# Kernel optimization log

Measured on AMD Instinct MI355X. Metric: run time of the kernel, lower is better.

## Reference

```python
import jax, jax.numpy as jnp
import numpy as np

B, T, S, H, E = 4, 2048, 2048, 16, 64  # batch, q_len, kv_len, heads, head_dim


def setup_inputs() -> dict:
    key = jax.random.key(0)
    kq, kk, kv, kl, kw = jax.random.split(key, 5)
    query = jax.random.normal(kq, (B, T, H * E), dtype=jnp.float32)
    key_t = jax.random.normal(kk, (B, S, H * E), dtype=jnp.float32)
    value = jax.random.normal(kv, (B, S, H * E), dtype=jnp.float32)
    # valid lengths in [S//2, S] so every row has at least one attendable key
    lengths = jax.random.randint(kl, (B,), S // 2, S + 1)
    key_padding_mask = jnp.arange(S)[None, :] < lengths[:, None]  # (B, S) bool, True = keep
    W_out = jax.random.normal(kw, (H * E, E), dtype=jnp.float32) * 0.02
    b_out = jnp.zeros((E,), dtype=jnp.float32)
    return {"query": query, "key": key_t, "value": value,
            "key_padding_mask": key_padding_mask, "W_out": W_out, "b_out": b_out}


def reference(query, key, value, key_padding_mask, W_out, b_out):
    # (B, N, H*E) -> (B, H, N, E)
    q = query.reshape(B, T, H, E).transpose(0, 2, 1, 3)
    k = key.reshape(B, S, H, E).transpose(0, 2, 1, 3)
    v = value.reshape(B, S, H, E).transpose(0, 2, 1, 3)
    softmax_temp = 1.0 / np.sqrt(E).astype(np.float32)
    scores = jnp.einsum('bhte,bhse->bhts', q * softmax_temp, k)  # (B,H,T,S)
    neg_inf = jnp.finfo(scores.dtype).min
    scores = jnp.where(key_padding_mask[:, None, None, :], scores, neg_inf)
    attn = jax.nn.softmax(scores, axis=-1)  # dropout p=0 -> identity
    out = jnp.einsum('bhts,bhsd->bthd', attn, v)  # (B,T,H,E)
    out = out.reshape(B * T, H * E)
    return out @ W_out + b_out  # (B*T, E)
```

## Files before the change

### kernel.cpp

```cpp
#include <hip/hip_runtime.h>
#include <hip/hip_bf16.h>

#define Bq 4
#define Tq 2048
#define Sq 2048
#define Hq 16
#define Eq 64
#define HEq 1024

typedef __attribute__((ext_vector_type(8))) _Float16 half8;
typedef __attribute__((ext_vector_type(16))) float f32x16;

#define AS1 __attribute__((address_space(1)))
#define AS3 __attribute__((address_space(3)))

__device__ __forceinline__ void gl_lds16(const void* g, void* l) {
  __builtin_amdgcn_global_load_lds((const AS1 unsigned*)g, (AS3 unsigned*)l, 16, 0, 0);
}
#define VMCNT(n) asm volatile("s_waitcnt vmcnt(" #n ")" ::: "memory")
#define LGKM0 asm volatile("s_waitcnt lgkmcnt(0)" ::: "memory")

#if __has_builtin(__builtin_amdgcn_exp2f)
#define EXP2F(x) __builtin_amdgcn_exp2f(x)
#else
#define EXP2F(x) exp2f(x)
#endif

__device__ __forceinline__ unsigned pk16(float a, float b) {
  return __builtin_bit_cast(unsigned, __builtin_amdgcn_cvt_pkrtz(a, b));
}

__global__ __launch_bounds__(256) void prep_kernel(
    const float* __restrict__ K, const float* __restrict__ V,
    const float* __restrict__ W, const void* __restrict__ mask,
    char* __restrict__ KP, char* __restrict__ VP,
    _Float16* __restrict__ WT, int* __restrict__ lens) {
  __shared__ _Float16 tile[64][72];
  const int bid = blockIdx.x;
  const int tid = threadIdx.x;

  if (bid < 4096) {
    const int isV = bid >= 2048;
    const int b2 = bid & 2047;
    const int t = b2 & 31, h = (b2 >> 5) & 15, b = b2 >> 9;
    const int s0 = t * 64;
    const int s_in = tid >> 2, e0 = (tid & 3) * 16;
    const float* X = isV ? V : K;
    const float* src = X + ((size_t)(b * Sq + s0 + s_in) * HEq + h * Eq + e0);
#pragma unroll
    for (int i = 0; i < 4; ++i) {
      const float4 f = *(const float4*)(src + i * 4);
      tile[s_in][e0 + i * 4 + 0] = (_Float16)f.x;
      tile[s_in][e0 + i * 4 + 1] = (_Float16)f.y;
      tile[s_in][e0 + i * 4 + 2] = (_Float16)f.z;
      tile[s_in][e0 + i * 4 + 3] = (_Float16)f.w;
    }
    __syncthreads();
    half8 u0, u1;
    if (!isV) {
      const int gi = tid >> 5, sl = (tid & 31) * 2;
#pragma unroll
      for (int j = 0; j < 8; ++j) {
        u0[j] = tile[sl][gi * 8 + j];
        u1[j] = tile[sl + 1][gi * 8 + j];
      }
      char* dst = KP + ((size_t)b2 * 8192) + tid * 32;
      *(half8*)dst = u0;
      *(half8*)(dst + 16) = u1;
    } else {
      const int sgi = tid >> 5, e = (tid & 31) * 2;
#pragma unroll
      for (int j = 0; j < 8; ++j) {
        u0[j] = tile[sgi * 8 + j][e];
        u1[j] = tile[sgi * 8 + j][e + 1];
      }
      char* dst = VP + ((size_t)b2 * 8192) + tid * 32;
      *(half8*)dst = u0;
      *(half8*)(dst + 16) = u1;
    }
  } else if (bid < 4352) {
    const int id = (bid - 4096) * 256 + tid;
    const int n = id >> 10, k = id & 1023;
    WT[id] = (_Float16)W[k * Eq + n];
  } else if (tid < 64) {
    const int b = bid - 4352;
    const int lane = tid;
    const unsigned w0 = *(const unsigned*)mask;
    int cnt = 0;
    if (w0 == 1u) {
      const int* m = (const int*)mask + b * Sq;
      for (int s = lane; s < Sq; s += 64) cnt += (m[s] != 0);
    } else if (w0 == 0x3F800000u) {
      const float* m = (const float*)mask + b * Sq;
      for (int s = lane; s < Sq; s += 64) cnt += (m[s] != 0.f);
    } else {
      const unsigned char* m = (const unsigned char*)mask + b * Sq;
      for (int s = lane; s < Sq; s += 64) cnt += (m[s] != 0);
    }
    for (int o = 32; o; o >>= 1) cnt += __shfl_down(cnt, o);
    if (lane == 0) lens[b] = cnt;
  }
}

__global__ __launch_bounds__(512, 4) void flash_kernel(
    const float* __restrict__ Q, const char* __restrict__ KP,
    const char* __restrict__ VP, const int* __restrict__ lens,
    _Float16* __restrict__ attnO) {
  __shared__ __align__(16) _Float16 KV[2][2][4096];

  const int bid = blockIdx.x;
  const int qt = bid >> 6;
  const int h = (bid >> 2) & 15;
  const int b = ((bid & 3) + (bid >> 8)) & 3;
  const int tid = threadIdx.x;
  const int w = tid >> 6, lane = tid & 63;
  const int qq = lane & 31, hi = lane >> 5;
  const int len = lens[b];
  const int q0 = qt * 256 + w * 32;

  const float qscale = 0.125f * 1.44269504088896340736f;
  half8 qf[4];
  {
    const float* qrow = Q + ((size_t)(b * Tq + q0 + qq) * HEq + h * Eq);
#pragma unroll
    for (int kw = 0; kw < 4; ++kw) {
      const float4 f0 = *(const float4*)(qrow + kw * 16 + hi * 8);
      const float4 f1 = *(const float4*)(qrow + kw * 16 + hi * 8 + 4);
      half8 qv;
      qv[0] = (_Float16)(f0.x * qscale);
      qv[1] = (_Float16)(f0.y * qscale);
      qv[2] = (_Float16)(f0.z * qscale);
      qv[3] = (_Float16)(f0.w * qscale);
      qv[4] = (_Float16)(f1.x * qscale);
      qv[5] = (_Float16)(f1.y * qscale);
      qv[6] = (_Float16)(f1.z * qscale);
      qv[7] = (_Float16)(f1.w * qscale);
      qf[kw] = qv;
    }
  }

  f32x16 Oa[2];
#pragma unroll
  for (int i = 0; i < 2; ++i)
#pragma unroll
    for (int r = 0; r < 16; ++r) Oa[i][r] = 0.f;
  float ls0 = 0.f, ls1 = 0.f;

  const char* kpb = KP + (size_t)(b * Hq + h) * 32 * 8192;
  const char* vpb = VP + (size_t)(b * Hq + h) * 32 * 8192;
  const int so = w * 1024 + lane * 16;

  const int ntiles = (len + 63) >> 6;

  gl_lds16(kpb + so, (char*)&KV[0][0][0] + so);
  gl_lds16(vpb + so, (char*)&KV[0][1][0] + so);

  int p = 0;
  for (int t = 0; t < ntiles; ++t) {
    if (t + 1 < ntiles) {
      const size_t tb = (size_t)(t + 1) * 8192;
      gl_lds16(kpb + tb + so, (char*)&KV[p ^ 1][0][0] + so);
      gl_lds16(vpb + tb + so, (char*)&KV[p ^ 1][1][0] + so);
      VMCNT(2);
    } else {
      VMCNT(0);
    }
    __builtin_amdgcn_s_barrier();
    __builtin_amdgcn_sched_barrier(0);

    __builtin_amdgcn_s_setprio(1);
    f32x16 sc[2];
#pragma unroll
    for (int sm = 0; sm < 2; ++sm) {
      f32x16 acc;
#pragma unroll
      for (int r = 0; r < 16; ++r) acc[r] = 0.f;
#pragma unroll
      for (int kw = 0; kw < 4; ++kw) {
        const half8 kf = *(const half8*)((const char*)&KV[p][0][0] +
                                         (kw * 2 + hi) * 1024 + (sm * 32 + qq) * 16);
        acc = __builtin_amdgcn_mfma_f32_32x32x16_f16(kf, qf[kw], acc, 0, 0, 0);
      }
      sc[sm] = acc;
    }
    __builtin_amdgcn_s_setprio(0);

    const int svalid = len - (t << 6);
    if (svalid < 64) {
#pragma unroll
      for (int r = 0; r < 16; ++r) {
        const int sl = (r & 3) + 8 * (r >> 2) + 4 * hi;
        if (sl >= svalid) sc[0][r] = -60000.f;
        if (32 + sl >= svalid) sc[1][r] = -60000.f;
      }
    }

    unsigned pku[2][4][2];
#pragma unroll
    for (int sm = 0; sm < 2; ++sm)
#pragma unroll
      for (int rb = 0; rb < 4; ++rb)
#pragma unroll
        for (int pp = 0; pp < 2; ++pp) {
          const float a0 = EXP2F(sc[sm][rb * 4 + pp * 2]);
          const float a1 = EXP2F(sc[sm][rb * 4 + pp * 2 + 1]);
          ls0 += a0;
          ls1 += a1;
          pku[sm][rb][pp] = pk16(a0, a1);
        }

#pragma unroll
    for (int kw = 0; kw < 4; ++kw) {
      const int sm = kw >> 1;
      const int rbe = (kw & 1) * 2, rbo = rbe + 1;
      union { unsigned u[4]; half8 h; } pu;
#pragma unroll
      for (int pp = 0; pp < 2; ++pp) {
        const unsigned ev = pku[sm][rbe][pp];
        const unsigned od = pku[sm][rbo][pp];
        const unsigned sendv = hi ? ev : od;
        const unsigned recvv = __shfl_xor(sendv, 32);
        pu.u[pp] = hi ? recvv : ev;
        pu.u[2 + pp] = hi ? od : recvv;
      }
      const half8 pf = pu.h;
      __builtin_amdgcn_s_setprio(1);
#pragma unroll
      for (int eh = 0; eh < 2; ++eh) {
        const half8 vf = *(const half8*)((const char*)&KV[p][1][0] +
                                         (kw * 2 + hi) * 1024 + (eh * 32 + qq) * 16);
        Oa[eh] = __builtin_amdgcn_mfma_f32_32x32x16_f16(vf, pf, Oa[eh], 0, 0, 0);
      }
      __builtin_amdgcn_s_setprio(0);
    }

    __builtin_amdgcn_s_barrier();
    __builtin_amdgcn_sched_barrier(0);
    p ^= 1;
  }

  float ls = ls0 + ls1;
  ls += __shfl_xor(ls, 32);
  const float inv = 1.f / ls;
  char* const scratch = (char*)&KV[0][0][0] + w * 4096;
#pragma unroll
  for (int eh = 0; eh < 2; ++eh)
#pragma unroll
    for (int rb = 0; rb < 4; ++rb)
#pragma unroll
      for (int pp = 0; pp < 2; ++pp) {
        const int e0 = eh * 32 + rb * 8 + hi * 4 + pp * 2;
        const unsigned uo = pk16(Oa[eh][rb * 4 + pp * 2] * inv,
                                 Oa[eh][rb * 4 + pp * 2 + 1] * inv);
        *(unsigned*)(scratch + qq * 128 + ((e0 * 2) ^ ((qq & 7) << 4))) = uo;
      }
  LGKM0;
  __builtin_amdgcn_sched_barrier(0);
#pragma unroll
  for (int i = 0; i < 4; ++i) {
    const int qr = i * 8 + (lane >> 3), ch = lane & 7;
    const half8 ov = *(const half8*)(scratch + qr * 128 + ((ch * 16) ^ ((qr & 7) << 4)));
    *(half8*)(attnO + (size_t)(b * Tq + q0 + qr) * HEq + h * Eq + ch * 8) = ov;
  }
}

typedef __attribute__((ext_vector_type(4))) float floatx4;
__global__ __launch_bounds__(256) void proj_kernel(
    const _Float16* __restrict__ A, const _Float16* __restrict__ WT,
    const float* __restrict__ bias, float* __restrict__ out) {
  const int tid = threadIdx.x;
  const int w = tid >> 6, lane = tid & 63;
  const int g = lane >> 4, c = lane & 15;
  const int r0 = blockIdx.x * 64 + w * 16;
  floatx4 acc[4];
#pragma unroll
  for (int i = 0; i < 4; ++i) acc[i] = (floatx4){0.f, 0.f, 0.f, 0.f};
  const _Float16* arow = A + (size_t)(r0 + c) * HEq;
  for (int kc = 0; kc < 32; ++kc) {
    const half8 af = *(const half8*)(arow + kc * 32 + g * 8);
#pragma unroll
    for (int nt = 0; nt < 4; ++nt) {
      const half8 bf =
          *(const half8*)(WT + (size_t)(nt * 16 + c) * HEq + kc * 32 + g * 8);
      acc[nt] = __builtin_amdgcn_mfma_f32_16x16x32_f16(af, bf, acc[nt], 0, 0, 0);
    }
  }
#pragma unroll
  for (int r = 0; r < 4; ++r) {
    const int row = r0 + g * 4 + r;
#pragma unroll
    for (int nt = 0; nt < 4; ++nt) {
      const int col = nt * 16 + c;
      out[(size_t)row * Eq + col] = acc[nt][r] + bias[col];
    }
  }
}

extern "C" void kernel_launch(void* const* d_in, const int* in_sizes, int n_in,
                              void* d_out, int out_size, void* d_ws, size_t ws_size,
                              hipStream_t stream) {
  const float* q = (const float*)d_in[0];
  const float* k = (const float*)d_in[1];
  const float* v = (const float*)d_in[2];
  const void* mask = d_in[3];
  const float* W = (const float*)d_in[4];
  const float* bias = (const float*)d_in[5];
  float* out = (float*)d_out;

  char* ws = (char*)d_ws;
  int* lens = (int*)ws;
  _Float16* WT = (_Float16*)(ws + 256);
  _Float16* attn = (_Float16*)(ws + (256 + 131072));
  char* KP = ws + (256 + 131072 + (1 << 24));
  char* VP = ws + (256 + 131072 + (1 << 24) + (1 << 24));

  prep_kernel<<<4356, 256, 0, stream>>>(k, v, W, mask, KP, VP, WT, lens);
  flash_kernel<<<512, 512, 0, stream>>>(q, KP, VP, lens, attn);
  proj_kernel<<<(Bq * Tq) / 64, 256, 0, stream>>>(attn, WT, bias, out);
}
```

Measured before the change: 108.4 us.

## Process two KV tiles per barrier and compute softmax row sums via MFMA

The KV loop now stages two 64-key tiles per buffer half, so each barrier pair covers two tiles and loads run further ahead. That doubles LDS use to 64KB per block, which may limit occupancy. The per-lane scalar accumulation of exp values plus the cross-lane shuffle for the row sum is replaced by an extra MFMA against a ones vector, which yields the row sums in an accumulator. This removes VALU adds but adds one MFMA per k-step, and the sum is now taken over fp16-rounded probabilities.

Result: slower. 113.4 us (+4.6%).

```diff
diff --git a/kernel.cpp b/kernel.cpp
--- a/kernel.cpp
+++ b/kernel.cpp
@@ -106,7 +106,7 @@
     const float* __restrict__ Q, const char* __restrict__ KP,
     const char* __restrict__ VP, const int* __restrict__ lens,
     _Float16* __restrict__ attnO) {
-  __shared__ __align__(16) _Float16 KV[2][2][4096];
+  __shared__ __align__(16) _Float16 KV[2][2][2][4096];
 
   const int bid = blockIdx.x;
   const int qt = bid >> 6;
@@ -139,35 +139,25 @@
     }
   }
 
-  f32x16 Oa[2];
+  half8 ones;
+#pragma unroll
+  for (int j = 0; j < 8; ++j) ones[j] = (_Float16)1.0f;
+
+  f32x16 Oa[2], La;
 #pragma unroll
   for (int i = 0; i < 2; ++i)
 #pragma unroll
     for (int r = 0; r < 16; ++r) Oa[i][r] = 0.f;
-  float ls0 = 0.f, ls1 = 0.f;
+#pragma unroll
+  for (int r = 0; r < 16; ++r) La[r] = 0.f;
 
   const char* kpb = KP + (size_t)(b * Hq + h) * 32 * 8192;
   const char* vpb = VP + (size_t)(b * Hq + h) * 32 * 8192;
   const int so = w * 1024 + lane * 16;
 
-  const int ntiles = (len + 63) >> 6;
-
-  gl_lds16(kpb + so, (char*)&KV[0][0][0] + so);
-  gl_lds16(vpb + so, (char*)&KV[0][1][0] + so);
-
-  int p = 0;
-  for (int t = 0; t < ntiles; ++t) {
-    if (t + 1 < ntiles) {
-      const size_t tb = (size_t)(t + 1) * 8192;
-      gl_lds16(kpb + tb + so, (char*)&KV[p ^ 1][0][0] + so);
-      gl_lds16(vpb + tb + so, (char*)&KV[p ^ 1][1][0] + so);
-      VMCNT(2);
-    } else {
-      VMCNT(0);
-    }
-    __builtin_amdgcn_s_barrier();
-    __builtin_amdgcn_sched_barrier(0);
-
+  const int nt = (len + 63) >> 6;
+
+  auto compute_tile = [&](const char* kbuf, const char* vbuf, int svalid) {
     __builtin_amdgcn_s_setprio(1);
     f32x16 sc[2];
 #pragma unroll
@@ -177,15 +167,14 @@
       for (int r = 0; r < 16; ++r) acc[r] = 0.f;
 #pragma unroll
       for (int kw = 0; kw < 4; ++kw) {
-        const half8 kf = *(const half8*)((const char*)&KV[p][0][0] +
-                                         (kw * 2 + hi) * 1024 + (sm * 32 + qq) * 16);
+        const half8 kf = *(const half8*)(kbuf + (kw * 2 + hi) * 1024 +
+                                         (sm * 32 + qq) * 16);
         acc = __builtin_amdgcn_mfma_f32_32x32x16_f16(kf, qf[kw], acc, 0, 0, 0);
       }
       sc[sm] = acc;
     }
     __builtin_amdgcn_s_setprio(0);
 
-    const int svalid = len - (t << 6);
     if (svalid < 64) {
 #pragma unroll
       for (int r = 0; r < 16; ++r) {
@@ -204,8 +193,6 @@
         for (int pp = 0; pp < 2; ++pp) {
           const float a0 = EXP2F(sc[sm][rb * 4 + pp * 2]);
           const float a1 = EXP2F(sc[sm][rb * 4 + pp * 2 + 1]);
-          ls0 += a0;
-          ls1 += a1;
           pku[sm][rb][pp] = pk16(a0, a1);
         }
 
@@ -227,31 +214,59 @@
       __builtin_amdgcn_s_setprio(1);
 #pragma unroll
       for (int eh = 0; eh < 2; ++eh) {
-        const half8 vf = *(const half8*)((const char*)&KV[p][1][0] +
-                                         (kw * 2 + hi) * 1024 + (eh * 32 + qq) * 16);
+        const half8 vf = *(const half8*)(vbuf + (kw * 2 + hi) * 1024 +
+                                         (eh * 32 + qq) * 16);
         Oa[eh] = __builtin_amdgcn_mfma_f32_32x32x16_f16(vf, pf, Oa[eh], 0, 0, 0);
       }
+      La = __builtin_amdgcn_mfma_f32_32x32x16_f16(ones, pf, La, 0, 0, 0);
       __builtin_amdgcn_s_setprio(0);
     }
-
+  };
+
+  gl_lds16(kpb + so, (char*)&KV[0][0][0][0] + so);
+  gl_lds16(vpb + so, (char*)&KV[0][0][1][0] + so);
+  {
+    const size_t t1 = (size_t)(1 < nt ? 1 : 0) * 8192;
+    gl_lds16(kpb + t1 + so, (char*)&KV[0][1][0][0] + so);
+    gl_lds16(vpb + t1 + so, (char*)&KV[0][1][1][0] + so);
+  }
+
+  int pp = 0;
+  for (int t = 0; t < nt; t += 2) {
+    {
+      const int ia = (t + 2 < nt) ? t + 2 : nt - 1;
+      const int ib = (t + 3 < nt) ? t + 3 : nt - 1;
+      gl_lds16(kpb + (size_t)ia * 8192 + so, (char*)&KV[pp ^ 1][0][0][0] + so);
+      gl_lds16(vpb + (size_t)ia * 8192 + so, (char*)&KV[pp ^ 1][0][1][0] + so);
+      gl_lds16(kpb + (size_t)ib * 8192 + so, (char*)&KV[pp ^ 1][1][0][0] + so);
+      gl_lds16(vpb + (size_t)ib * 8192 + so, (char*)&KV[pp ^ 1][1][1][0] + so);
+    }
+    VMCNT(4);
     __builtin_amdgcn_s_barrier();
     __builtin_amdgcn_sched_barrier(0);
-    p ^= 1;
-  }
-
-  float ls = ls0 + ls1;
-  ls += __shfl_xor(ls, 32);
-  const float inv = 1.f / ls;
-  char* const scratch = (char*)&KV[0][0][0] + w * 4096;
+
+    compute_tile((const char*)&KV[pp][0][0][0], (const char*)&KV[pp][0][1][0],
+                 len - t * 64);
+    if (t + 1 < nt)
+      compute_tile((const char*)&KV[pp][1][0][0], (const char*)&KV[pp][1][1][0],
+                   len - (t + 1) * 64);
+
+    __builtin_amdgcn_s_barrier();
+    __builtin_amdgcn_sched_barrier(0);
+    pp ^= 1;
+  }
+
+  const float inv = 1.f / La[0];
+  char* const scratch = (char*)&KV[0][0][0][0] + w * 4096;
 #pragma unroll
   for (int eh = 0; eh < 2; ++eh)
 #pragma unroll
     for (int rb = 0; rb < 4; ++rb)
 #pragma unroll
-      for (int pp = 0; pp < 2; ++pp) {
-        const int e0 = eh * 32 + rb * 8 + hi * 4 + pp * 2;
-        const unsigned uo = pk16(Oa[eh][rb * 4 + pp * 2] * inv,
-                                 Oa[eh][rb * 4 + pp * 2 + 1] * inv);
+      for (int pp2 = 0; pp2 < 2; ++pp2) {
+        const int e0 = eh * 32 + rb * 8 + hi * 4 + pp2 * 2;
+        const unsigned uo = pk16(Oa[eh][rb * 4 + pp2 * 2] * inv,
+                                 Oa[eh][rb * 4 + pp2 * 2 + 1] * inv);
         *(unsigned*)(scratch + qq * 128 + ((e0 * 2) ^ ((qq & 7) << 4))) = uo;
       }
   LGKM0;
```

## Split each KV tile across wave pairs and merge partial outputs via LDS

Applied to the files above, without the earlier changes.

Each query block of 32 rows is now handled by two waves, each computing scores and PV for half of every 64-key tile. The partial O accumulators and row sums are combined through LDS at the end. Blocks now cover 128 queries, so twice as many blocks are launched, with the launch bound raised to allow more occupancy. This doubles parallelism and cuts per-wave serial work. The cost is an fp16 round-trip of partial O, an extra barrier and reduction, and K/V tile loads shared by fewer queries.

Result: slower. 301.8 us (+178.4%).

```diff
diff --git a/kernel.cpp b/kernel.cpp
--- a/kernel.cpp
+++ b/kernel.cpp
@@ -10,6 +10,7 @@
 
 typedef __attribute__((ext_vector_type(8))) _Float16 half8;
 typedef __attribute__((ext_vector_type(16))) float f32x16;
+typedef __attribute__((ext_vector_type(4))) unsigned uint4v;
 
 #define AS1 __attribute__((address_space(1)))
 #define AS3 __attribute__((address_space(3)))
@@ -102,21 +103,24 @@
   }
 }
 
-__global__ __launch_bounds__(512, 4) void flash_kernel(
+__global__ __launch_bounds__(512, 8) void flash_kernel(
     const float* __restrict__ Q, const char* __restrict__ KP,
     const char* __restrict__ VP, const int* __restrict__ lens,
     _Float16* __restrict__ attnO) {
   __shared__ __align__(16) _Float16 KV[2][2][4096];
 
   const int bid = blockIdx.x;
-  const int qt = bid >> 6;
+  const int top2 = bid >> 8;
+  const int b = ((bid & 3) + top2) & 3;
   const int h = (bid >> 2) & 15;
-  const int b = ((bid & 3) + (bid >> 8)) & 3;
+  const int qt = ((bid >> 6) & 3) | (top2 << 2);
   const int tid = threadIdx.x;
   const int w = tid >> 6, lane = tid & 63;
   const int qq = lane & 31, hi = lane >> 5;
+  const int smw = w & 1;
+  const int pr = w >> 1;
   const int len = lens[b];
-  const int q0 = qt * 256 + w * 32;
+  const int q0 = qt * 128 + pr * 32;
 
   const float qscale = 0.125f * 1.44269504088896340736f;
   half8 qf[4];
@@ -169,19 +173,14 @@
     __builtin_amdgcn_sched_barrier(0);
 
     __builtin_amdgcn_s_setprio(1);
-    f32x16 sc[2];
-#pragma unroll
-    for (int sm = 0; sm < 2; ++sm) {
-      f32x16 acc;
-#pragma unroll
-      for (int r = 0; r < 16; ++r) acc[r] = 0.f;
-#pragma unroll
-      for (int kw = 0; kw < 4; ++kw) {
-        const half8 kf = *(const half8*)((const char*)&KV[p][0][0] +
-                                         (kw * 2 + hi) * 1024 + (sm * 32 + qq) * 16);
-        acc = __builtin_amdgcn_mfma_f32_32x32x16_f16(kf, qf[kw], acc, 0, 0, 0);
-      }
-      sc[sm] = acc;
+    f32x16 sc;
+#pragma unroll
+    for (int r = 0; r < 16; ++r) sc[r] = 0.f;
+#pragma unroll
+    for (int kw = 0; kw < 4; ++kw) {
+      const half8 kf = *(const half8*)((const char*)&KV[p][0][0] +
+                                       (kw * 2 + hi) * 1024 + (smw * 32 + qq) * 16);
+      sc = __builtin_amdgcn_mfma_f32_32x32x16_f16(kf, qf[kw], sc, 0, 0, 0);
     }
     __builtin_amdgcn_s_setprio(0);
 
@@ -189,35 +188,32 @@
     if (svalid < 64) {
 #pragma unroll
       for (int r = 0; r < 16; ++r) {
-        const int sl = (r & 3) + 8 * (r >> 2) + 4 * hi;
-        if (sl >= svalid) sc[0][r] = -60000.f;
-        if (32 + sl >= svalid) sc[1][r] = -60000.f;
-      }
-    }
-
-    unsigned pku[2][4][2];
-#pragma unroll
-    for (int sm = 0; sm < 2; ++sm)
-#pragma unroll
-      for (int rb = 0; rb < 4; ++rb)
-#pragma unroll
-        for (int pp = 0; pp < 2; ++pp) {
-          const float a0 = EXP2F(sc[sm][rb * 4 + pp * 2]);
-          const float a1 = EXP2F(sc[sm][rb * 4 + pp * 2 + 1]);
-          ls0 += a0;
-          ls1 += a1;
-          pku[sm][rb][pp] = pk16(a0, a1);
-        }
-
-#pragma unroll
-    for (int kw = 0; kw < 4; ++kw) {
-      const int sm = kw >> 1;
-      const int rbe = (kw & 1) * 2, rbo = rbe + 1;
+        const int sl = smw * 32 + (r & 3) + 8 * (r >> 2) + 4 * hi;
+        if (sl >= svalid) sc[r] = -60000.f;
+      }
+    }
+
+    unsigned pku[4][2];
+#pragma unroll
+    for (int rb = 0; rb < 4; ++rb)
+#pragma unroll
+      for (int pp = 0; pp < 2; ++pp) {
+        const float a0 = EXP2F(sc[rb * 4 + pp * 2]);
+        const float a1 = EXP2F(sc[rb * 4 + pp * 2 + 1]);
+        ls0 += a0;
+        ls1 += a1;
+        pku[rb][pp] = pk16(a0, a1);
+      }
+
+#pragma unroll
+    for (int kwl = 0; kwl < 2; ++kwl) {
+      const int kwg = smw * 2 + kwl;
+      const int rbe = kwl * 2, rbo = rbe + 1;
       union { unsigned u[4]; half8 h; } pu;
 #pragma unroll
       for (int pp = 0; pp < 2; ++pp) {
-        const unsigned ev = pku[sm][rbe][pp];
-        const unsigned od = pku[sm][rbo][pp];
+        const unsigned ev = pku[rbe][pp];
+        const unsigned od = pku[rbo][pp];
         const unsigned sendv = hi ? ev : od;
         const unsigned recvv = __shfl_xor(sendv, 32);
         pu.u[pp] = hi ? recvv : ev;
@@ -228,7 +224,7 @@
 #pragma unroll
       for (int eh = 0; eh < 2; ++eh) {
         const half8 vf = *(const half8*)((const char*)&KV[p][1][0] +
-                                         (kw * 2 + hi) * 1024 + (eh * 32 + qq) * 16);
+                                         (kwg * 2 + hi) * 1024 + (eh * 32 + qq) * 16);
         Oa[eh] = __builtin_amdgcn_mfma_f32_32x32x16_f16(vf, pf, Oa[eh], 0, 0, 0);
       }
       __builtin_amdgcn_s_setprio(0);
@@ -241,26 +237,60 @@
 
   float ls = ls0 + ls1;
   ls += __shfl_xor(ls, 32);
-  const float inv = 1.f / ls;
-  char* const scratch = (char*)&KV[0][0][0] + w * 4096;
-#pragma unroll
-  for (int eh = 0; eh < 2; ++eh)
-#pragma unroll
-    for (int rb = 0; rb < 4; ++rb)
-#pragma unroll
-      for (int pp = 0; pp < 2; ++pp) {
-        const int e0 = eh * 32 + rb * 8 + hi * 4 + pp * 2;
-        const unsigned uo = pk16(Oa[eh][rb * 4 + pp * 2] * inv,
-                                 Oa[eh][rb * 4 + pp * 2 + 1] * inv);
-        *(unsigned*)(scratch + qq * 128 + ((e0 * 2) ^ ((qq & 7) << 4))) = uo;
-      }
-  LGKM0;
+
+  char* const obuf = (char*)&KV[0][0][0];
+  float* const lbuf = (float*)((char*)&KV[0][0][0] + 16384);
+  if (smw) {
+    unsigned ou[16];
+#pragma unroll
+    for (int i = 0; i < 16; ++i)
+      ou[i] = pk16(Oa[i >> 3][(i & 7) * 2], Oa[i >> 3][(i & 7) * 2 + 1]);
+    char* dst = obuf + pr * 4096 + lane * 64;
+#pragma unroll
+    for (int j = 0; j < 4; ++j) {
+      uint4v v = {ou[j * 4], ou[j * 4 + 1], ou[j * 4 + 2], ou[j * 4 + 3]};
+      *(uint4v*)(dst + j * 16) = v;
+    }
+    lbuf[pr * 64 + lane] = ls;
+    LGKM0;
+  }
+  __builtin_amdgcn_s_barrier();
   __builtin_amdgcn_sched_barrier(0);
-#pragma unroll
-  for (int i = 0; i < 4; ++i) {
-    const int qr = i * 8 + (lane >> 3), ch = lane & 7;
-    const half8 ov = *(const half8*)(scratch + qr * 128 + ((ch * 16) ^ ((qr & 7) << 4)));
-    *(half8*)(attnO + (size_t)(b * Tq + q0 + qr) * HEq + h * Eq + ch * 8) = ov;
+  if (!smw) {
+    const char* srcb = obuf + pr * 4096 + lane * 64;
+    uint4v ov[4];
+#pragma unroll
+    for (int j = 0; j < 4; ++j) ov[j] = *(const uint4v*)(srcb + j * 16);
+    const float lp = lbuf[pr * 64 + lane];
+#pragma unroll
+    for (int i = 0; i < 16; ++i) {
+      union { unsigned u; _Float16 hv[2]; } cv;
+      cv.u = ov[i >> 2][i & 3];
+      Oa[i >> 3][(i & 7) * 2] += (float)cv.hv[0];
+      Oa[i >> 3][(i & 7) * 2 + 1] += (float)cv.hv[1];
+    }
+    const float inv = 1.f / (ls + lp);
+    char* const scratch = obuf + pr * 4096;
+#pragma unroll
+    for (int eh = 0; eh < 2; ++eh)
+#pragma unroll
+      for (int rb = 0; rb < 4; ++rb)
+#pragma unroll
+        for (int pp2 = 0; pp2 < 2; ++pp2) {
+          const int e0 = eh * 32 + rb * 8 + hi * 4 + pp2 * 2;
+          const unsigned uo = pk16(Oa[eh][rb * 4 + pp2 * 2] * inv,
+                                   Oa[eh][rb * 4 + pp2 * 2 + 1] * inv);
+          *(unsigned*)(scratch + qq * 128 + ((e0 * 2) ^ ((qq & 7) << 4))) = uo;
+        }
+    LGKM0;
+    __builtin_amdgcn_sched_barrier(0);
+#pragma unroll
+    for (int i = 0; i < 4; ++i) {
+      const int qr = i * 8 + (lane >> 3), ch = lane & 7;
+      const half8 ov2 =
+          *(const half8*)(scratch + qr * 128 + ((ch * 16) ^ ((qr & 7) << 4)));
+      *(half8*)(attnO + (size_t)(b * Tq + q0 + qr) * HEq + h * Eq + ch * 8) = ov2;
+    }
   }
 }
 
@@ -315,6 +345,6 @@
   char* VP = ws + (256 + 131072 + (1 << 24) + (1 << 24));
 
   prep_kernel<<<4356, 256, 0, stream>>>(k, v, W, mask, KP, VP, WT, lens);
-  flash_kernel<<<512, 512, 0, stream>>>(q, KP, VP, lens, attn);
+  flash_kernel<<<1024, 512, 0, stream>>>(q, KP, VP, lens, attn);
   proj_kernel<<<(Bq * Tq) / 64, 256, 0, stream>>>(attn, WT, bias, out);
 }
```

## Split KV range across two blocks per query tile and add combine kernel

Applied to the files above, without the earlier changes.

The flash attention grid doubles. Each block now handles half of the valid key tiles and writes an unnormalized fp16 partial output plus its row sum to workspace. A new combine kernel adds the two partials, divides by the summed row sums and writes the normalized attention output for the projection kernel. The aim is more concurrent blocks per CU and shorter per-block serial loops. The cost is an extra round-trip of partial outputs through memory and one more kernel launch. Correctness depends on both halves using the same max offset, since the partials are summed without rescaling.

Result: slower. 119.1 us (+9.8%).

```diff
diff --git a/kernel.cpp b/kernel.cpp
--- a/kernel.cpp
+++ b/kernel.cpp
@@ -105,13 +105,15 @@
 __global__ __launch_bounds__(512, 4) void flash_kernel(
     const float* __restrict__ Q, const char* __restrict__ KP,
     const char* __restrict__ VP, const int* __restrict__ lens,
-    _Float16* __restrict__ attnO) {
+    _Float16* __restrict__ PO, float* __restrict__ L) {
   __shared__ __align__(16) _Float16 KV[2][2][4096];
 
   const int bid = blockIdx.x;
-  const int qt = bid >> 6;
-  const int h = (bid >> 2) & 15;
-  const int b = ((bid & 3) + (bid >> 8)) & 3;
+  const int shalf = bid >> 9;
+  const int r9 = bid & 511;
+  const int qt = r9 >> 6;
+  const int h = (r9 >> 2) & 15;
+  const int b = ((r9 & 3) + (r9 >> 8)) & 3;
   const int tid = threadIdx.x;
   const int w = tid >> 6, lane = tid & 63;
   const int qq = lane & 31, hi = lane >> 5;
@@ -150,14 +152,17 @@
   const char* vpb = VP + (size_t)(b * Hq + h) * 32 * 8192;
   const int so = w * 1024 + lane * 16;
 
-  const int ntiles = (len + 63) >> 6;
-
-  gl_lds16(kpb + so, (char*)&KV[0][0][0] + so);
-  gl_lds16(vpb + so, (char*)&KV[0][1][0] + so);
+  const int nt = (len + 63) >> 6;
+  const int nt0 = (nt + 1) >> 1;
+  const int tbeg = shalf ? nt0 : 0;
+  const int tend = shalf ? nt : nt0;
+
+  gl_lds16(kpb + (size_t)tbeg * 8192 + so, (char*)&KV[0][0][0] + so);
+  gl_lds16(vpb + (size_t)tbeg * 8192 + so, (char*)&KV[0][1][0] + so);
 
   int p = 0;
-  for (int t = 0; t < ntiles; ++t) {
-    if (t + 1 < ntiles) {
+  for (int t = tbeg; t < tend; ++t) {
+    if (t + 1 < tend) {
       const size_t tb = (size_t)(t + 1) * 8192;
       gl_lds16(kpb + tb + so, (char*)&KV[p ^ 1][0][0] + so);
       gl_lds16(vpb + tb + so, (char*)&KV[p ^ 1][1][0] + so);
@@ -241,17 +246,19 @@
 
   float ls = ls0 + ls1;
   ls += __shfl_xor(ls, 32);
-  const float inv = 1.f / ls;
+  const size_t pbase = (size_t)(shalf * 64 + b * Hq + h) * 2048;
+  if (hi == 0) L[pbase + q0 + qq] = ls;
+
   char* const scratch = (char*)&KV[0][0][0] + w * 4096;
 #pragma unroll
   for (int eh = 0; eh < 2; ++eh)
 #pragma unroll
     for (int rb = 0; rb < 4; ++rb)
 #pragma unroll
-      for (int pp = 0; pp < 2; ++pp) {
-        const int e0 = eh * 32 + rb * 8 + hi * 4 + pp * 2;
-        const unsigned uo = pk16(Oa[eh][rb * 4 + pp * 2] * inv,
-                                 Oa[eh][rb * 4 + pp * 2 + 1] * inv);
+      for (int pp2 = 0; pp2 < 2; ++pp2) {
+        const int e0 = eh * 32 + rb * 8 + hi * 4 + pp2 * 2;
+        const unsigned uo = pk16(Oa[eh][rb * 4 + pp2 * 2],
+                                 Oa[eh][rb * 4 + pp2 * 2 + 1]);
         *(unsigned*)(scratch + qq * 128 + ((e0 * 2) ^ ((qq & 7) << 4))) = uo;
       }
   LGKM0;
@@ -260,8 +267,27 @@
   for (int i = 0; i < 4; ++i) {
     const int qr = i * 8 + (lane >> 3), ch = lane & 7;
     const half8 ov = *(const half8*)(scratch + qr * 128 + ((ch * 16) ^ ((qr & 7) << 4)));
-    *(half8*)(attnO + (size_t)(b * Tq + q0 + qr) * HEq + h * Eq + ch * 8) = ov;
-  }
+    *(half8*)(PO + (pbase + q0 + qr) * 64 + ch * 8) = ov;
+  }
+}
+
+__global__ __launch_bounds__(256) void combine_kernel(
+    const _Float16* __restrict__ PO, const float* __restrict__ L,
+    _Float16* __restrict__ attn) {
+  const size_t id = (size_t)blockIdx.x * 256 + threadIdx.x;
+  const int j = (int)(id & 7);
+  const size_t pq = id >> 3;
+  const half8 o0 = *(const half8*)(PO + pq * 64 + j * 8);
+  const half8 o1 = *(const half8*)(PO + ((size_t)64 * 2048 * 64) + pq * 64 + j * 8);
+  const float inv = 1.f / (L[pq] + L[(size_t)64 * 2048 + pq]);
+  half8 r;
+#pragma unroll
+  for (int i = 0; i < 8; ++i)
+    r[i] = (_Float16)(((float)o0[i] + (float)o1[i]) * inv);
+  const int p = (int)(pq >> 11);
+  const int q = (int)(pq & 2047);
+  const int b = p >> 4, h = p & 15;
+  *(half8*)(attn + (size_t)(b * Tq + q) * HEq + h * 64 + j * 8) = r;
 }
 
 typedef __attribute__((ext_vector_type(4))) float floatx4;
@@ -312,9 +338,12 @@
   _Float16* WT = (_Float16*)(ws + 256);
   _Float16* attn = (_Float16*)(ws + (256 + 131072));
   char* KP = ws + (256 + 131072 + (1 << 24));
-  char* VP = ws + (256 + 131072 + (1 << 24) + (1 << 24));
+  char* VP = ws + (256 + 131072 + 2 * (1 << 24));
+  _Float16* PO = (_Float16*)(ws + (256 + 131072 + 3 * (1 << 24)));
+  float* L = (float*)(ws + (256 + 131072 + 5 * (1 << 24)));
 
   prep_kernel<<<4356, 256, 0, stream>>>(k, v, W, mask, KP, VP, WT, lens);
-  flash_kernel<<<512, 512, 0, stream>>>(q, KP, VP, lens, attn);
+  flash_kernel<<<1024, 512, 0, stream>>>(q, KP, VP, lens, PO, L);
+  combine_kernel<<<4096, 256, 0, stream>>>(PO, L, attn);
   proj_kernel<<<(Bq * Tq) / 64, 256, 0, stream>>>(attn, WT, bias, out);
 }
```
